# Kernel tuning notes

Measured on AMD Instinct MI355X. Metric: run time of the kernel, lower is better.

Reference implementation:

```python
import jax, jax.numpy as jnp
import numpy as np

N = 20000      # atoms
E = 240000     # edges (avg degree ~12, matches _AVG_DEGREE_MATPES)
C = 128        # sphere_channels
ZMAX = 100     # max_num_elements
NG = 600       # GaussianSmearing(0, cutoff, 600, 2.0)
CUTOFF = 6.0
WIDTH = 2.0    # basis_width_scalar
RESCALE = 12.0 # _AVG_DEGREE_MATPES
LN_EPS = 1e-5
# xyz -> (y,z,x): real-SH component order for l=1, so Wigner D^(1) = P R P^T
P = np.array([[0.,1.,0.],[0.,0.,1.],[1.,0.,0.]], dtype=np.float32)


def _layernorm(x, g, b):
    mu = jnp.mean(x, axis=-1, keepdims=True)
    var = jnp.mean((x - mu) ** 2, axis=-1, keepdims=True)
    return g * (x - mu) * jax.lax.rsqrt(var + LN_EPS) + b


def init_edge_rot_mat(ev):
    # faithful port of init_edge_rot_mat (torch uses .detach())
    ev = jax.lax.stop_gradient(ev)
    dist = jnp.maximum(jnp.linalg.norm(ev, axis=1, keepdims=True), 1e-8)
    nx = ev / dist
    ref = jnp.eye(3, dtype=ev.dtype)[jnp.argmin(jnp.abs(nx), axis=1)]
    nz = jnp.cross(nx, ref)
    nz = nz / jnp.maximum(jnp.linalg.norm(nz, axis=1, keepdims=True), 1e-8)
    ny = jnp.cross(nx, nz)
    ny = ny / jnp.maximum(jnp.linalg.norm(ny, axis=1, keepdims=True), 1e-8)
    # edge_rot_mat_inv has columns [nz, nx, -ny]; rot = inv^T -> rows [nz, nx, -ny]
    return jnp.stack([nz, nx, -ny], axis=1)  # [E,3,3]


def setup_inputs() -> dict:
    key = jax.random.key(0)
    ks = jax.random.split(key, 10)
    s = 0.02
    return {
        'edge_distance_vec': jax.random.normal(ks[0], (E, 3), jnp.float32) * 2.0,
        'sphere_emb': jax.random.normal(ks[1], (ZMAX, C), jnp.float32) * s,
        'src_emb': jax.random.normal(ks[2], (ZMAX, C), jnp.float32) * s,
        'tgt_emb': jax.random.normal(ks[3], (ZMAX, C), jnp.float32) * s,
        'W1': jax.random.normal(ks[4], (NG + 2 * C, C), jnp.float32) * s,
        'b1': jnp.zeros((C,), jnp.float32),
        'g1': jnp.ones((C,), jnp.float32),
        'be1': jnp.zeros((C,), jnp.float32),
        'W2': jax.random.normal(ks[5], (C, C), jnp.float32) * s,
        'b2': jnp.zeros((C,), jnp.float32),
        'g2': jnp.ones((C,), jnp.float32),
        'be2': jnp.zeros((C,), jnp.float32),
        'W3': jax.random.normal(ks[6], (C, 2 * C), jnp.float32) * s,
        'b3': jnp.zeros((2 * C,), jnp.float32),
        'atomic_numbers': jax.random.randint(ks[7], (N,), 0, ZMAX),
        'edge_index': jax.random.randint(ks[8], (2, E), 0, N),
    }


def reference(edge_distance_vec, sphere_emb, src_emb, tgt_emb,
              W1, b1, g1, be1, W2, b2, g2, be2, W3, b3,
              atomic_numbers, edge_index):
    src, dst = edge_index[0], edge_index[1]
    Pm = jnp.asarray(P)
    # per-edge rotation to edge-aligned frame and its l=1 Wigner matrix
    rot = init_edge_rot_mat(edge_distance_vec)               # [E,3,3]
    D1 = jnp.einsum('ij,ejk,lk->eil', Pm, rot, Pm)           # [E,3,3]
    # Gaussian distance expansion (600 basis fns)
    dist = jnp.linalg.norm(edge_distance_vec, axis=1)        # [E]
    offsets = jnp.linspace(0.0, CUTOFF, NG)
    coeff = -0.5 / (WIDTH * (offsets[1] - offsets[0])) ** 2
    gauss = jnp.exp(coeff * (dist[:, None] - offsets[None, :]) ** 2)  # [E,600]
    # edge features: distance basis + source/target atom embeddings
    x_edge = jnp.concatenate(
        [gauss, src_emb[atomic_numbers[src]], tgt_emb[atomic_numbers[dst]]], axis=1)
    # RadialFunction: Linear->LN->SiLU x2, final Linear -> m=0 coefficients
    h = jax.nn.silu(_layernorm(x_edge @ W1 + b1, g1, be1))
    h = jax.nn.silu(_layernorm(h @ W2 + b2, g2, be2))
    m0 = (h @ W3 + b3).reshape(E, 2, C)   # (l=0,m=0) and (l=1,m=0)
    # rotate back to global frame: blockdiag(1, D1)^T applied to (m0[0]; 0, m0[1], 0)
    l0 = m0[:, 0][:, None, :]                                 # [E,1,C]
    l1 = jnp.einsum('ei,ec->eic', D1[:, 1, :], m0[:, 1])      # (D1^T v)_i with v=(0,a,0)
    msg = jnp.concatenate([l0, l1], axis=1)                   # [E,4,C]
    # scatter-sum messages to target nodes, rescale by avg degree
    x_deg = jnp.zeros((N, 4, C), msg.dtype).at[dst].add(msg) / RESCALE
    # node init: atom embedding into l=0 slot, plus edge-degree embedding
    x = x_deg.at[:, 0].add(sphere_emb[atomic_numbers])
    return x
```

## Files before the change

kernel.cpp:

```cpp
#include <hip/hip_runtime.h>
#include <stdint.h>

#define EE 240000
#define NN 20000
#define NB 4096

typedef __attribute__((ext_vector_type(4))) float f32x4;
typedef __attribute__((ext_vector_type(8))) __bf16 bf16x8;
typedef __attribute__((ext_vector_type(8))) short s16x8;

union V8 { s16x8 s; bf16x8 b; uint4 u; };

static constexpr float GC2 =
    (float)((-0.5 / ((12.0 / 599.0) * (12.0 / 599.0))) * 1.4426950408889634);

__device__ __forceinline__ float b2f(unsigned short u) {
    return __uint_as_float(((unsigned)u) << 16);
}
__device__ __forceinline__ unsigned short f2b(float f) {
    unsigned u = __float_as_uint(f);
    return (unsigned short)((u + 0x7fffu + ((u >> 16) & 1u)) >> 16);
}
__device__ __forceinline__ unsigned cvtpk(float lo, float hi) {
    unsigned r;
    asm("v_cvt_pk_bf16_f32 %0, %1, %2" : "=v"(r) : "v"(lo), "v"(hi));
    return r;
}
__device__ __forceinline__ unsigned short ldc(const void* p, int i, bool isb) {
    return isb ? ((const unsigned short*)p)[i] : f2b(((const float*)p)[i]);
}
__device__ __forceinline__ float ldf(const void* p, int i, bool isb) {
    return isb ? b2f(((const unsigned short*)p)[i]) : ((const float*)p)[i];
}
__device__ __forceinline__ bool probe_isb(const void* g1) {
    return ((const unsigned*)g1)[0] != 0x3F800000u;
}

__device__ __forceinline__ int kperm(int p) {
    int wi = p >> 1;
    return ((wi >> 4) << 5) + (wi & 15) + ((p & 1) << 4);
}

#define PREP_PARAMS_TOTAL (77824 + 16384 + 32768 + 6400 + 6400 + 1024)
#define PB ((PREP_PARAMS_TOTAL + 255) / 256)
#define EB ((EE + 255) / 256)

__global__ void prep_all(const void* ev, const int* __restrict__ an,
                         const int* __restrict__ ei,
                         const void* W1, const void* W2, const void* W3,
                         const void* se, const void* te,
                         const void* b1, const void* g1, const void* be1,
                         const void* b2, const void* g2, const void* be2,
                         const void* b3,
                         unsigned short* __restrict__ W1T,
                         unsigned short* __restrict__ W2T,
                         unsigned short* __restrict__ W3T,
                         float2* __restrict__ SEWT,
                         float2* __restrict__ TEWT,
                         unsigned short* __restrict__ vecs,
                         uint4* __restrict__ sedge_u, float4* __restrict__ d1_out,
                         int* __restrict__ deg, int* __restrict__ bhist) {
    bool isb = probe_isb(g1);
    int bid = blockIdx.x;
    if (bid < PB) {
        int t = bid * 256 + threadIdx.x;
        if (t < 77824) {
            int j = t & 7, n = (t >> 3) & 127, kb = t >> 10;
            int k = kb * 8 + j;
            W1T[t] = (k < 600) ? ldc(W1, k * 128 + n, isb) : (unsigned short)0;
            return;
        }
        t -= 77824;
        if (t < 16384) {
            int j = t & 7, n = (t >> 3) & 127, kb = t >> 10;
            W2T[t] = ldc(W2, kperm(kb * 8 + j) * 128 + n, isb);
            return;
        }
        t -= 16384;
        if (t < 32768) {
            int j = t & 7, n = (t >> 3) & 255, kb = t >> 11;
            W3T[t] = ldc(W3, kperm(kb * 8 + j) * 256 + n, isb);
            return;
        }
        t -= 32768;
        if (t < 6400) {
            int z = t >> 6, wi = t & 63;
            int c0 = ((wi >> 4) << 5) | (wi & 15), c1 = c0 + 16;
            float a0 = ldf(b1, c0, isb), a1 = ldf(b1, c1, isb);
            for (int k = 0; k < 128; ++k) {
                float sv = ldf(se, z * 128 + k, isb);
                a0 += sv * ldf(W1, (600 + k) * 128 + c0, isb);
                a1 += sv * ldf(W1, (600 + k) * 128 + c1, isb);
            }
            float2 w; w.x = a0; w.y = a1;
            SEWT[t] = w;
            return;
        }
        t -= 6400;
        if (t < 6400) {
            int z = t >> 6, wi = t & 63;
            int c0 = ((wi >> 4) << 5) | (wi & 15), c1 = c0 + 16;
            float a0 = 0.f, a1 = 0.f;
            for (int k = 0; k < 128; ++k) {
                float tv = ldf(te, z * 128 + k, isb);
                a0 += tv * ldf(W1, (728 + k) * 128 + c0, isb);
                a1 += tv * ldf(W1, (728 + k) * 128 + c1, isb);
            }
            float2 w; w.x = a0; w.y = a1;
            TEWT[t] = w;
            return;
        }
        t -= 6400;
        if (t < 128) { vecs[t] = ldc(b1, t, isb); return; }
        t -= 128;
        if (t < 128) { vecs[128 + t] = ldc(g1, t, isb); return; }
        t -= 128;
        if (t < 128) { vecs[256 + t] = ldc(be1, t, isb); return; }
        t -= 128;
        if (t < 128) { vecs[384 + t] = ldc(b2, t, isb); return; }
        t -= 128;
        if (t < 128) { vecs[512 + t] = ldc(g2, t, isb); return; }
        t -= 128;
        if (t < 128) { vecs[640 + t] = ldc(be2, t, isb); return; }
        t -= 128;
        if (t < 256) { vecs[768 + t] = ldc(b3, t, isb); return; }
        return;
    }
    int e = (bid - PB) * 256 + threadIdx.x;
    if (e >= EE) return;
    float x = ldf(ev, e * 3 + 0, isb);
    float y = ldf(ev, e * 3 + 1, isb);
    float z = ldf(ev, e * 3 + 2, isb);
    float nrm = sqrtf(x * x + y * y + z * z);
    float dc = fmaxf(nrm, 1e-8f);
    float nx0 = x / dc, nx1 = y / dc, nx2 = z / dc;
    float a0 = fabsf(nx0), a1 = fabsf(nx1), a2 = fabsf(nx2);
    int idx = 0; float mv = a0;
    if (a1 < mv) { idx = 1; mv = a1; }
    if (a2 < mv) { idx = 2; }
    float r0 = (idx == 0) ? 1.f : 0.f;
    float r1 = (idx == 1) ? 1.f : 0.f;
    float r2 = (idx == 2) ? 1.f : 0.f;
    float z0 = nx1 * r2 - nx2 * r1;
    float z1 = nx2 * r0 - nx0 * r2;
    float z2 = nx0 * r1 - nx1 * r0;
    float zn = fmaxf(sqrtf(z0 * z0 + z1 * z1 + z2 * z2), 1e-8f);
    z0 /= zn; z1 /= zn; z2 /= zn;
    float y0 = nx1 * z2 - nx2 * z1;
    float y1 = nx2 * z0 - nx0 * z2;
    float y2 = nx0 * z1 - nx1 * z0;
    float yn = fmaxf(sqrtf(y0 * y0 + y1 * y1 + y2 * y2), 1e-8f);
    y0 /= yn; y1 /= yn; y2 /= yn;
    float4 dv; dv.x = -y1; dv.y = -y2; dv.z = -y0; dv.w = 0.f;
    d1_out[e] = dv;
    int zsv = an[ei[e]];
    int dst = ei[EE + e];
    int zdv = an[dst];
    uint4 su;
    su.x = __float_as_uint(nrm);
    su.y = (unsigned)zsv | ((unsigned)zdv << 16);
    su.z = (unsigned)e;
    su.w = 0;
    sedge_u[e] = su;
    atomicAdd(&deg[dst], 1);
    int b = min(NB - 1, (int)(nrm * 512.0f));
    atomicAdd(&bhist[b], 1);
}

__global__ __launch_bounds__(1024) void scan_all(
    const int* __restrict__ deg, const int* __restrict__ bhist,
    int* __restrict__ row_start, int* __restrict__ cursor, int* __restrict__ bcursor) {
    __shared__ int lds[1024];
    int t = threadIdx.x;
    int base = t * 20;
    int loc[20]; int ls = 0;
#pragma unroll
    for (int j = 0; j < 20; ++j) {
        int i = base + j;
        ls += (i < NN) ? deg[i] : 0;
        loc[j] = ls;
    }
    lds[t] = ls; __syncthreads();
    for (int s = 1; s < 1024; s <<= 1) {
        int v = (t >= s) ? lds[t - s] : 0;
        __syncthreads(); lds[t] += v; __syncthreads();
    }
    int off = lds[t] - ls;
#pragma unroll
    for (int j = 0; j < 20; ++j) {
        int i = base + j;
        if (i < NN) {
            row_start[i + 1] = off + loc[j];
            cursor[i] = off + (j ? loc[j - 1] : 0);
        }
    }
    if (t == 0) row_start[0] = 0;
    __syncthreads();
    int b4 = t * 4;
    int l4[4]; int bs = 0;
#pragma unroll
    for (int j = 0; j < 4; ++j) { bs += bhist[b4 + j]; l4[j] = bs; }
    lds[t] = bs; __syncthreads();
    for (int s = 1; s < 1024; s <<= 1) {
        int v = (t >= s) ? lds[t - s] : 0;
        __syncthreads(); lds[t] += v; __syncthreads();
    }
    int boff = lds[t] - bs;
#pragma unroll
    for (int j = 0; j < 4; ++j) bcursor[b4 + j] = boff + (j ? l4[j - 1] : 0);
}

__global__ void fill_sorted(const int* __restrict__ ei,
                            const uint4* __restrict__ sedge_u,
                            const float4* __restrict__ d1v,
                            int* __restrict__ cursor, int* __restrict__ bcursor,
                            uint4* __restrict__ sedge_s, float4* __restrict__ d1s) {
    int e = blockIdx.x * 256 + threadIdx.x;
    if (e >= EE) return;
    uint4 su = sedge_u[e];
    int dst = ei[EE + e];
    int p = atomicAdd(&cursor[dst], 1);
    float d = __uint_as_float(su.x);
    int b = min(NB - 1, (int)(d * 512.0f));
    int sp = atomicAdd(&bcursor[b], 1);
    su.z = (unsigned)p;
    sedge_s[sp] = su;
    d1s[p] = d1v[e];
}

__device__ __forceinline__ void ln_silu(f32x4 (&acc)[2][8],
                                        const unsigned short* __restrict__ gamma,
                                        const unsigned short* __restrict__ beta,
                                        int i16, int quad,
                                        unsigned short (*ht)[136]) {
    float gm[8], bt[8];
#pragma unroll
    for (int nt = 0; nt < 8; ++nt) {
        gm[nt] = b2f(gamma[nt * 16 + i16]);
        bt[nt] = b2f(beta[nt * 16 + i16]);
    }
#pragma unroll
    for (int mt = 0; mt < 2; ++mt) {
#pragma unroll
        for (int r = 0; r < 4; ++r) {
            float s = 0.f, s2 = 0.f;
#pragma unroll
            for (int nt = 0; nt < 8; ++nt) {
                float v = acc[mt][nt][r];
                s += v; s2 += v * v;
            }
#pragma unroll
            for (int m = 1; m < 16; m <<= 1) {
                s += __shfl_xor(s, m);
                s2 += __shfl_xor(s2, m);
            }
            float mu = s * (1.f / 128.f);
            float var = s2 * (1.f / 128.f) - mu * mu;
            float rs = rsqrtf(var + 1e-5f);
            unsigned* wrow = (unsigned*)ht[mt * 16 + quad * 4 + r];
#pragma unroll
            for (int ntp = 0; ntp < 4; ++ntp) {
                float zz[2];
#pragma unroll
                for (int h = 0; h < 2; ++h) {
                    int nt = 2 * ntp + h;
                    float y = gm[nt] * (acc[mt][nt][r] - mu) * rs + bt[nt];
                    zz[h] = y * __builtin_amdgcn_rcpf(1.f + exp2f(-1.4426950409f * y));
                }
                wrow[ntp * 16 + i16] = cvtpk(zz[0], zz[1]);
            }
        }
    }
}

template <bool MSG>
__global__ __launch_bounds__(256, 4) void edge_mlp(
    const unsigned short* __restrict__ W1T, const unsigned short* __restrict__ W2T,
    const unsigned short* __restrict__ W3T,
    const float2* __restrict__ SEWT, const float2* __restrict__ TEWT,
    const unsigned short* __restrict__ vecs,
    const uint4* __restrict__ sedge,
    const int* __restrict__ ei, const float4* __restrict__ d1v,
    unsigned* __restrict__ msg, float* __restrict__ xacc) {
    __shared__ __align__(16) unsigned short htile_s[4][32][136];
    int tid = threadIdx.x;
    int wave = tid >> 6, lane = tid & 63;
    int i16 = lane & 15, quad = lane >> 4;
    unsigned short (*ht)[136] = htile_s[wave];
    int mbase = blockIdx.x * 128 + wave * 32;

    uint4 s0 = sedge[mbase + i16];
    uint4 s1 = sedge[mbase + 16 + i16];
    float dd0 = __uint_as_float(s0.x), dd1 = __uint_as_float(s1.x);
    int dpz0 = (int)s0.z, dpz1 = (int)s1.z;

    float dmn = fminf(dd0, dd1), dmx = fmaxf(dd0, dd1);
#pragma unroll
    for (int m = 1; m < 64; m <<= 1) {
        dmn = fminf(dmn, __shfl_xor(dmn, m));
        dmx = fmaxf(dmx, __shfl_xor(dmx, m));
    }
    int klo = (int)floorf((dmn - 0.285f) * (599.0f / 6.0f));
    int khi = (int)ceilf((dmx + 0.285f) * (599.0f / 6.0f));
    int ka = min(max(klo, 0) >> 5, 19);
    int kb = min((min(khi, 607) >> 5) + 1, 19);

    f32x4 acc[2][8];
#pragma unroll
    for (int mt = 0; mt < 2; ++mt) {
        unsigned sy = mt ? s1.y : s0.y;
#pragma unroll
        for (int r = 0; r < 4; ++r) {
            unsigned zy = (unsigned)__shfl((int)sy, quad * 4 + r);
            const float2* sw = SEWT + (zy & 0xFFFFu) * 64 + i16;
            const float2* tw = TEWT + (zy >> 16) * 64 + i16;
#pragma unroll
            for (int ntp = 0; ntp < 4; ++ntp) {
                float2 a = sw[ntp * 16];
                float2 b = tw[ntp * 16];
                acc[mt][2 * ntp][r]     = a.x + b.x;
                acc[mt][2 * ntp + 1][r] = a.y + b.y;
            }
        }
    }

#pragma unroll 1
    for (int ks = ka; ks < kb; ++ks) {
        int k0 = ks * 32 + quad * 8;
        V8 af[2];
#pragma unroll
        for (int mt = 0; mt < 2; ++mt) {
            float dm = mt ? dd1 : dd0;
            float e[8];
#pragma unroll
            for (int j = 0; j < 8; ++j) {
                float t = dm - (float)(k0 + j) * (6.0f / 599.0f);
                e[j] = exp2f(GC2 * t * t);
            }
            af[mt].u.x = cvtpk(e[0], e[1]);
            af[mt].u.y = cvtpk(e[2], e[3]);
            af[mt].u.z = cvtpk(e[4], e[5]);
            af[mt].u.w = cvtpk(e[6], e[7]);
        }
        const unsigned short* w1p = W1T + (((ks * 4 + quad) * 128 + i16) << 3);
#pragma unroll
        for (int nt = 0; nt < 8; ++nt) {
            V8 bf_; bf_.s = *(const s16x8*)(w1p + nt * 128);
            acc[0][nt] = __builtin_amdgcn_mfma_f32_16x16x32_bf16(af[0].b, bf_.b, acc[0][nt], 0, 0, 0);
            acc[1][nt] = __builtin_amdgcn_mfma_f32_16x16x32_bf16(af[1].b, bf_.b, acc[1][nt], 0, 0, 0);
        }
    }
    ln_silu(acc, vecs + 128, vecs + 256, i16, quad, ht);

#pragma unroll
    for (int mt = 0; mt < 2; ++mt)
#pragma unroll
        for (int nt = 0; nt < 8; ++nt) {
            float b = b2f(vecs[384 + nt * 16 + i16]);
#pragma unroll
            for (int q = 0; q < 4; ++q) acc[mt][nt][q] = b;
        }
#pragma unroll 1
    for (int ks = 0; ks < 4; ++ks) {
        int k0 = ks * 32 + quad * 8;
        V8 a0, a1;
        a0.s = *(const s16x8*)&ht[i16][k0];
        a1.s = *(const s16x8*)&ht[16 + i16][k0];
        const unsigned short* w2p = W2T + (((ks * 4 + quad) * 128 + i16) << 3);
#pragma unroll
        for (int nt = 0; nt < 8; ++nt) {
            V8 bf_; bf_.s = *(const s16x8*)(w2p + nt * 128);
            acc[0][nt] = __builtin_amdgcn_mfma_f32_16x16x32_bf16(a0.b, bf_.b, acc[0][nt], 0, 0, 0);
            acc[1][nt] = __builtin_amdgcn_mfma_f32_16x16x32_bf16(a1.b, bf_.b, acc[1][nt], 0, 0, 0);
        }
    }
    ln_silu(acc, vecs + 512, vecs + 640, i16, quad, ht);

#pragma unroll 1
    for (int half = 0; half < 2; ++half) {
#pragma unroll
        for (int mt = 0; mt < 2; ++mt)
#pragma unroll
            for (int nt = 0; nt < 8; ++nt) {
                float b = b2f(vecs[768 + half * 128 + nt * 16 + i16]);
#pragma unroll
                for (int q = 0; q < 4; ++q) acc[mt][nt][q] = b;
            }
#pragma unroll 1
        for (int ks = 0; ks < 4; ++ks) {
            int k0 = ks * 32 + quad * 8;
            V8 a0, a1;
            a0.s = *(const s16x8*)&ht[i16][k0];
            a1.s = *(const s16x8*)&ht[16 + i16][k0];
            const unsigned short* w3p = W3T + (((ks * 4 + quad) * 256 + half * 128 + i16) << 3);
#pragma unroll
            for (int nt = 0; nt < 8; ++nt) {
                V8 bf_; bf_.s = *(const s16x8*)(w3p + nt * 128);
                acc[0][nt] = __builtin_amdgcn_mfma_f32_16x16x32_bf16(a0.b, bf_.b, acc[0][nt], 0, 0, 0);
                acc[1][nt] = __builtin_amdgcn_mfma_f32_16x16x32_bf16(a1.b, bf_.b, acc[1][nt], 0, 0, 0);
            }
        }
        if constexpr (MSG) {
#pragma unroll
            for (int mt = 0; mt < 2; ++mt) {
                int dpz = mt ? dpz1 : dpz0;
#pragma unroll
                for (int r = 0; r < 4; ++r) {
                    int dp = __shfl(dpz, quad * 4 + r);
                    unsigned* mrow = msg + (size_t)dp * 128 + half * 64 + i16;
#pragma unroll
                    for (int ntp = 0; ntp < 4; ++ntp)
                        mrow[ntp * 16] = cvtpk(acc[mt][2 * ntp][r], acc[mt][2 * ntp + 1][r]);
                }
            }
        } else {
#pragma unroll
            for (int mt = 0; mt < 2; ++mt) {
#pragma unroll
                for (int r = 0; r < 4; ++r) {
                    int eidx = mbase + mt * 16 + quad * 4 + r;
                    int dn = ei[EE + eidx];
                    float* xb = xacc + (size_t)dn * 512;
                    if (half == 0) {
#pragma unroll
                        for (int nt = 0; nt < 8; ++nt)
                            atomicAdd(xb + nt * 16 + i16, acc[mt][nt][r]);
                    } else {
                        float4 dv = d1v[eidx];
#pragma unroll
                        for (int nt = 0; nt < 8; ++nt) {
                            float val = acc[mt][nt][r];
                            atomicAdd(xb + 128 + nt * 16 + i16, val * dv.x);
                            atomicAdd(xb + 256 + nt * 16 + i16, val * dv.y);
                            atomicAdd(xb + 384 + nt * 16 + i16, val * dv.z);
                        }
                    }
                }
            }
        }
    }
}

__global__ __launch_bounds__(256) void gather(
    const unsigned* __restrict__ msg,
    const float4* __restrict__ d1s, const int* __restrict__ row_start,
    const void* __restrict__ sp, const void* __restrict__ g1,
    const int* __restrict__ an, float* __restrict__ out) {
    __shared__ float cbuf[2][8][64];
    int tid = threadIdx.x;
    int w = tid >> 6, l = tid & 63;
    int nl = w >> 1, sub = w & 1;
    int n = blockIdx.x * 2 + nl;
    int c0 = ((l >> 4) << 5) | (l & 15);
    int i0 = row_start[n], i1 = row_start[n + 1];
    float a0 = 0.f, a1 = 0.f, x0 = 0.f, x1 = 0.f,
          y0 = 0.f, y1 = 0.f, z0 = 0.f, z1 = 0.f;
#pragma unroll 2
    for (int i = i0 + sub; i < i1; i += 2) {
        unsigned m0 = msg[(size_t)i * 128 + l];
        unsigned m1 = msg[(size_t)i * 128 + 64 + l];
        float4 dv = d1s[i];
        float p0 = b2f((unsigned short)m0), p1 = b2f((unsigned short)(m0 >> 16));
        float q0 = b2f((unsigned short)m1), q1 = b2f((unsigned short)(m1 >> 16));
        a0 += p0; a1 += p1;
        x0 += q0 * dv.x; x1 += q1 * dv.x;
        y0 += q0 * dv.y; y1 += q1 * dv.y;
        z0 += q0 * dv.z; z1 += q1 * dv.z;
    }
    if (sub) {
        cbuf[nl][0][l] = a0; cbuf[nl][1][l] = a1;
        cbuf[nl][2][l] = x0; cbuf[nl][3][l] = x1;
        cbuf[nl][4][l] = y0; cbuf[nl][5][l] = y1;
        cbuf[nl][6][l] = z0; cbuf[nl][7][l] = z1;
    }
    __syncthreads();
    if (!sub) {
        a0 += cbuf[nl][0][l]; a1 += cbuf[nl][1][l];
        x0 += cbuf[nl][2][l]; x1 += cbuf[nl][3][l];
        y0 += cbuf[nl][4][l]; y1 += cbuf[nl][5][l];
        z0 += cbuf[nl][6][l]; z1 += cbuf[nl][7][l];
        bool isb = probe_isb(g1);
        float* ob = out + (size_t)n * 512;
        int zb = an[n] * 128 + c0;
        constexpr float R = 1.f / 12.f;
        ob[c0]            = a0 * R + ldf(sp, zb, isb);
        ob[c0 + 16]       = a1 * R + ldf(sp, zb + 16, isb);
        ob[128 + c0]      = x0 * R;
        ob[128 + c0 + 16] = x1 * R;
        ob[256 + c0]      = y0 * R;
        ob[256 + c0 + 16] = y1 * R;
        ob[384 + c0]      = z0 * R;
        ob[384 + c0 + 16] = z1 * R;
    }
}

__global__ void finalize(const float* __restrict__ xacc, const void* __restrict__ sp,
                         const void* __restrict__ g1,
                         const int* __restrict__ an, float* __restrict__ out) {
    int t = blockIdx.x * 256 + threadIdx.x;
    bool isb = probe_isb(g1);
    int n = t >> 9, sc = t & 511;
    float v = xacc[t] * (1.f / 12.f);
    if (sc < 128) v += ldf(sp, an[n] * 128 + sc, isb);
    out[t] = v;
}

extern "C" void kernel_launch(void* const* d_in, const int* in_sizes, int n_in,
                              void* d_out, int out_size, void* d_ws, size_t ws_size,
                              hipStream_t stream) {
    const void* ev         = d_in[0];
    const void* sphere_emb = d_in[1];
    const void* src_emb    = d_in[2];
    const void* tgt_emb    = d_in[3];
    const void* W1  = d_in[4];  const void* b1  = d_in[5];
    const void* g1  = d_in[6];  const void* be1 = d_in[7];
    const void* W2  = d_in[8];  const void* b2  = d_in[9];
    const void* g2  = d_in[10]; const void* be2 = d_in[11];
    const void* W3  = d_in[12]; const void* b3  = d_in[13];
    const int* an   = (const int*)d_in[14];
    const int* ei   = (const int*)d_in[15];

    char* ws = (char*)d_ws;
    const size_t NEED_MSG = 132000000;

    if (ws_size >= NEED_MSG) {
        size_t off = 0;
        unsigned* msg = (unsigned*)(ws + off); off += (size_t)EE * 512;
        uint4* sedge_u = (uint4*)(ws + 0);
        float4* d1v    = (float4*)(ws + 3840000);
        float4* d1s    = (float4*)(ws + off);  off += (size_t)EE * 16;
        uint4* sedge_s = (uint4*)(ws + off);   off += (size_t)EE * 16;
        int* deg       = (int*)(ws + off);     off += (size_t)NN * 4;
        int* bhist     = (int*)(ws + off);     off += NB * 4;
        int* row_start = (int*)(ws + off);     off += (size_t)(NN + 4) * 4;
        int* cursor    = (int*)(ws + off);     off += (size_t)NN * 4;
        int* bcursor   = (int*)(ws + off);     off += NB * 4;
        unsigned short* W1T = (unsigned short*)(ws + off); off += 77824 * 2;
        unsigned short* W2T = (unsigned short*)(ws + off); off += 128 * 128 * 2;
        unsigned short* W3T = (unsigned short*)(ws + off); off += 256 * 128 * 2;
        float2* SEWT   = (float2*)(ws + off);  off += 6400 * 8;
        float2* TEWT   = (float2*)(ws + off);  off += 6400 * 8;
        unsigned short* vecs = (unsigned short*)(ws + off); off += 1024 * 2;

        hipMemsetAsync(deg, 0, (size_t)(NN + NB) * 4, stream);
        prep_all<<<PB + EB, 256, 0, stream>>>(
            ev, an, ei, W1, W2, W3, src_emb, tgt_emb,
            b1, g1, be1, b2, g2, be2, b3,
            W1T, W2T, W3T, SEWT, TEWT, vecs, sedge_u, d1v, deg, bhist);
        scan_all<<<1, 1024, 0, stream>>>(deg, bhist, row_start, cursor, bcursor);
        fill_sorted<<<(EE + 255) / 256, 256, 0, stream>>>(
            ei, sedge_u, d1v, cursor, bcursor, sedge_s, d1s);
        edge_mlp<true><<<EE / 128, 256, 0, stream>>>(
            W1T, W2T, W3T, SEWT, TEWT, vecs, sedge_s,
            (const int*)nullptr, (const float4*)nullptr, msg, (float*)nullptr);
        gather<<<NN / 2, 256, 0, stream>>>(msg, d1s, row_start,
                                           sphere_emb, g1, an, (float*)d_out);
    } else {
        size_t off = 0;
        float* xacc    = (float*)(ws + off);   off += (size_t)NN * 512 * 4;
        uint4* sedge_u = (uint4*)(ws + off);   off += (size_t)EE * 16;
        float4* d1v    = (float4*)(ws + off);  off += (size_t)EE * 16;
        int* deg       = (int*)(ws + off);     off += (size_t)NN * 4;
        int* bhist     = (int*)(ws + off);     off += NB * 4;
        unsigned short* W1T = (unsigned short*)(ws + off); off += 77824 * 2;
        unsigned short* W2T = (unsigned short*)(ws + off); off += 128 * 128 * 2;
        unsigned short* W3T = (unsigned short*)(ws + off); off += 256 * 128 * 2;
        float2* SEWT   = (float2*)(ws + off);  off += 6400 * 8;
        float2* TEWT   = (float2*)(ws + off);  off += 6400 * 8;
        unsigned short* vecs = (unsigned short*)(ws + off); off += 1024 * 2;

        hipMemsetAsync(xacc, 0, (size_t)NN * 512 * 4, stream);
        hipMemsetAsync(deg, 0, (size_t)(NN + NB) * 4, stream);
        prep_all<<<PB + EB, 256, 0, stream>>>(
            ev, an, ei, W1, W2, W3, src_emb, tgt_emb,
            b1, g1, be1, b2, g2, be2, b3,
            W1T, W2T, W3T, SEWT, TEWT, vecs, sedge_u, d1v, deg, bhist);
        edge_mlp<false><<<EE / 128, 256, 0, stream>>>(
            W1T, W2T, W3T, SEWT, TEWT, vecs, sedge_u, ei, d1v,
            (unsigned*)nullptr, xacc);
        finalize<<<(NN * 512) / 256, 256, 0, stream>>>(xacc, sphere_emb, g1, an,
                                                       (float*)d_out);
    }
}
```

Measured before the change: 338.9 us.

## Compute Gaussian basis by multiplicative recurrence and parallelize prep reductions and scans

Replaces eight exp2 evaluations per 8-wide Gaussian chunk with two exp2 calls plus a geometric-ratio recurrence of multiplies. Splits the per-element embedding projection in the prep kernel across four lanes, combined with shuffle reductions. Rewrites the block scans as wave-level shuffle scans with a small LDS pass, removing about twenty barriers per scan. The recurrence adds some rounding drift across the eight terms, which is mostly hidden by the bf16 conversion.

```diff
diff --git a/kernel.cpp b/kernel.cpp
--- a/kernel.cpp
+++ b/kernel.cpp
@@ -11,8 +11,12 @@
 
 union V8 { s16x8 s; bf16x8 b; uint4 u; };
 
-static constexpr float GC2 =
-    (float)((-0.5 / ((12.0 / 599.0) * (12.0 / 599.0))) * 1.4426950408889634);
+static constexpr double DD_ = 6.0 / 599.0;
+static constexpr double L2E_ = 1.4426950408889634;
+static constexpr float GC2 = (float)((-0.5 / (4.0 * DD_ * DD_)) * L2E_);
+static constexpr float RC0  = (float)((-0.5 / 4.0) * L2E_);
+static constexpr float RLIN = (float)(2.0 * (-0.5 / (4.0 * DD_ * DD_)) * L2E_ * DD_);
+static constexpr float QC   = (float)0.7788007830714049;
 
 __device__ __forceinline__ float b2f(unsigned short u) {
     return __uint_as_float(((unsigned)u) << 16);
@@ -41,7 +45,7 @@
     return ((wi >> 4) << 5) + (wi & 15) + ((p & 1) << 4);
 }
 
-#define PREP_PARAMS_TOTAL (77824 + 16384 + 32768 + 6400 + 6400 + 1024)
+#define PREP_PARAMS_TOTAL (77824 + 16384 + 32768 + 25600 + 25600 + 1024)
 #define PB ((PREP_PARAMS_TOTAL + 255) / 256)
 #define EB ((EE + 255) / 256)
 
@@ -83,34 +87,48 @@
             return;
         }
         t -= 32768;
-        if (t < 6400) {
-            int z = t >> 6, wi = t & 63;
+        if (t < 25600) {
+            int word = t >> 2, sub = t & 3;
+            int z = word >> 6, wi = word & 63;
             int c0 = ((wi >> 4) << 5) | (wi & 15), c1 = c0 + 16;
-            float a0 = ldf(b1, c0, isb), a1 = ldf(b1, c1, isb);
-            for (int k = 0; k < 128; ++k) {
+            float a0 = 0.f, a1 = 0.f;
+            int k0 = sub * 32;
+            for (int k = k0; k < k0 + 32; ++k) {
                 float sv = ldf(se, z * 128 + k, isb);
                 a0 += sv * ldf(W1, (600 + k) * 128 + c0, isb);
                 a1 += sv * ldf(W1, (600 + k) * 128 + c1, isb);
             }
-            float2 w; w.x = a0; w.y = a1;
-            SEWT[t] = w;
+            a0 += __shfl_xor(a0, 1); a0 += __shfl_xor(a0, 2);
+            a1 += __shfl_xor(a1, 1); a1 += __shfl_xor(a1, 2);
+            if (sub == 0) {
+                float2 w;
+                w.x = a0 + ldf(b1, c0, isb);
+                w.y = a1 + ldf(b1, c1, isb);
+                SEWT[word] = w;
+            }
             return;
         }
-        t -= 6400;
-        if (t < 6400) {
-            int z = t >> 6, wi = t & 63;
+        t -= 25600;
+        if (t < 25600) {
+            int word = t >> 2, sub = t & 3;
+            int z = word >> 6, wi = word & 63;
             int c0 = ((wi >> 4) << 5) | (wi & 15), c1 = c0 + 16;
             float a0 = 0.f, a1 = 0.f;
-            for (int k = 0; k < 128; ++k) {
+            int k0 = sub * 32;
+            for (int k = k0; k < k0 + 32; ++k) {
                 float tv = ldf(te, z * 128 + k, isb);
                 a0 += tv * ldf(W1, (728 + k) * 128 + c0, isb);
                 a1 += tv * ldf(W1, (728 + k) * 128 + c1, isb);
             }
-            float2 w; w.x = a0; w.y = a1;
-            TEWT[t] = w;
+            a0 += __shfl_xor(a0, 1); a0 += __shfl_xor(a0, 2);
+            a1 += __shfl_xor(a1, 1); a1 += __shfl_xor(a1, 2);
+            if (sub == 0) {
+                float2 w; w.x = a0; w.y = a1;
+                TEWT[word] = w;
+            }
             return;
         }
-        t -= 6400;
+        t -= 25600;
         if (t < 128) { vecs[t] = ldc(b1, t, isb); return; }
         t -= 128;
         if (t < 128) { vecs[128 + t] = ldc(g1, t, isb); return; }
@@ -170,8 +188,9 @@
 __global__ __launch_bounds__(1024) void scan_all(
     const int* __restrict__ deg, const int* __restrict__ bhist,
     int* __restrict__ row_start, int* __restrict__ cursor, int* __restrict__ bcursor) {
-    __shared__ int lds[1024];
+    __shared__ int lds[17];
     int t = threadIdx.x;
+    int lane = t & 63, wid = t >> 6;
     int base = t * 20;
     int loc[20]; int ls = 0;
 #pragma unroll
@@ -180,12 +199,19 @@
         ls += (i < NN) ? deg[i] : 0;
         loc[j] = ls;
     }
-    lds[t] = ls; __syncthreads();
-    for (int s = 1; s < 1024; s <<= 1) {
-        int v = (t >= s) ? lds[t - s] : 0;
-        __syncthreads(); lds[t] += v; __syncthreads();
-    }
-    int off = lds[t] - ls;
+    int x = ls;
+#pragma unroll
+    for (int s = 1; s < 64; s <<= 1) { int v = __shfl_up(x, s); if (lane >= s) x += v; }
+    if (lane == 63) lds[wid] = x;
+    __syncthreads();
+    if (wid == 0) {
+        int w = (lane < 16) ? lds[lane] : 0;
+#pragma unroll
+        for (int s = 1; s < 16; s <<= 1) { int v = __shfl_up(w, s); if (lane >= s) w += v; }
+        if (lane < 16) lds[lane] = w;
+    }
+    __syncthreads();
+    int off = (wid ? lds[wid - 1] : 0) + x - ls;
 #pragma unroll
     for (int j = 0; j < 20; ++j) {
         int i = base + j;
@@ -200,12 +226,19 @@
     int l4[4]; int bs = 0;
 #pragma unroll
     for (int j = 0; j < 4; ++j) { bs += bhist[b4 + j]; l4[j] = bs; }
-    lds[t] = bs; __syncthreads();
-    for (int s = 1; s < 1024; s <<= 1) {
-        int v = (t >= s) ? lds[t - s] : 0;
-        __syncthreads(); lds[t] += v; __syncthreads();
-    }
-    int boff = lds[t] - bs;
+    x = bs;
+#pragma unroll
+    for (int s = 1; s < 64; s <<= 1) { int v = __shfl_up(x, s); if (lane >= s) x += v; }
+    if (lane == 63) lds[wid] = x;
+    __syncthreads();
+    if (wid == 0) {
+        int w = (lane < 16) ? lds[lane] : 0;
+#pragma unroll
+        for (int s = 1; s < 16; s <<= 1) { int v = __shfl_up(w, s); if (lane >= s) w += v; }
+        if (lane < 16) lds[lane] = w;
+    }
+    __syncthreads();
+    int boff = (wid ? lds[wid - 1] : 0) + x - bs;
 #pragma unroll
     for (int j = 0; j < 4; ++j) bcursor[b4 + j] = boff + (j ? l4[j - 1] : 0);
 }
@@ -331,16 +364,20 @@
 #pragma unroll
         for (int mt = 0; mt < 2; ++mt) {
             float dm = mt ? dd1 : dd0;
-            float e[8];
-#pragma unroll
-            for (int j = 0; j < 8; ++j) {
-                float t = dm - (float)(k0 + j) * (6.0f / 599.0f);
-                e[j] = exp2f(GC2 * t * t);
-            }
-            af[mt].u.x = cvtpk(e[0], e[1]);
-            af[mt].u.y = cvtpk(e[2], e[3]);
-            af[mt].u.z = cvtpk(e[4], e[5]);
-            af[mt].u.w = cvtpk(e[6], e[7]);
+            float t0 = dm - (float)k0 * (float)(6.0 / 599.0);
+            float e0 = exp2f(GC2 * t0 * t0);
+            float r = exp2f(fmaf(-RLIN, t0, RC0));
+            float e1 = e0 * r; r *= QC;
+            float e2 = e1 * r; r *= QC;
+            float e3 = e2 * r; r *= QC;
+            float e4 = e3 * r; r *= QC;
+            float e5 = e4 * r; r *= QC;
+            float e6 = e5 * r; r *= QC;
+            float e7 = e6 * r;
+            af[mt].u.x = cvtpk(e0, e1);
+            af[mt].u.y = cvtpk(e2, e3);
+            af[mt].u.z = cvtpk(e4, e5);
+            af[mt].u.w = cvtpk(e6, e7);
         }
         const unsigned short* w1p = W1T + (((ks * 4 + quad) * 128 + i16) << 3);
 #pragma unroll
```

After: 313.1 us. -7.6%, faster.
